# Kernel tuning notes

Hardware: AMD Instinct MI355X
Metric: run time of the kernel (lower is better)

The kernel has to match this reference:

```python
import jax, jax.numpy as jnp
import numpy as np

B, L, U, G, H = 64, 110, 768, 512, 256
WP = WF = 10
NSP = 2
R = 2 * NSP * NSP      # 8 relation types
NB = 30                # RGCN num_bases
FF = 2048              # torch TransformerEncoderLayer default dim_feedforward
TAG = 7
N = B * L
NEG = -1e9


def _build_edges():
    # static windowed edge structure (all dialogues have length L)
    js, ks = [], []
    for j in range(L):
        for k in range(max(0, j - WP), min(L - 1, j + WF) + 1):
            js.append(j); ks.append(k)
    j = np.asarray(js, np.int32); k = np.asarray(ks, np.int32)
    c = (j >= k).astype(np.int32)  # edge_type suffix: '0' if j<k else '1'
    off = (np.arange(B, dtype=np.int32) * L)[:, None]
    src = (j[None, :] + off).reshape(-1)
    dst = (k[None, :] + off).reshape(-1)
    return src, dst, np.tile(k, B), np.tile(c, B)


def _ln(x, g, b):
    m = x.mean(-1, keepdims=True)
    v = ((x - m) ** 2).mean(-1, keepdims=True)
    return (x - m) / jnp.sqrt(v + 1e-5) * g + b


def _core(x, in_proj_w, in_proj_b, out_proj_w, out_proj_b, ln1_g, ln1_b,
          ff1_w, ff1_b, ff2_w, ff2_b, ln2_g, ln2_b, to_w, to_b, att_w,
          rgcn_basis, rgcn_comp, rgcn_root, rgcn_bias,
          gc_rel_w, gc_rel_b, gc_root_w, clf1_w, clf1_b, clf2_w, clf2_b,
          speaker, src, dst, k_local, cflag):
    # --- SeqContext: 1-layer, 1-head post-norm transformer (eval mode) ---
    qkv = x @ in_proj_w.T + in_proj_b
    q, kk, v = jnp.split(qkv, 3, axis=-1)
    attn = jax.nn.softmax(jnp.einsum('bqd,bkd->bqk', q, kk) / jnp.sqrt(jnp.float32(U)), -1)
    a = jnp.einsum('bqk,bkd->bqd', attn, v) @ out_proj_w.T + out_proj_b
    h = _ln(x + a, ln1_g, ln1_b)
    ff = jax.nn.relu(h @ ff1_w.T + ff1_b) @ ff2_w.T + ff2_b
    h = _ln(h + ff, ln2_g, ln2_b)
    feats = h @ to_w.T + to_b                      # (B, L, G) node features

    # --- EdgeAtt: windowed softmax attention, score[j,k] = x_j^T W x_k ---
    scores = jnp.einsum('bjd,de,bke->bjk', feats, att_w, feats)
    rel = jnp.arange(L)[None, :] - jnp.arange(L)[:, None]
    mask = (rel >= -WP) & (rel <= WF)
    alpha = jax.nn.softmax(jnp.where(mask[None], scores, NEG), -1)  # (B, L, L)

    xf = feats.reshape(N, G)
    edge_norm = alpha.reshape(N, L)[src, k_local]   # alpha[b, j, k] per edge

    # --- edge types from speakers: idx = (s1*NSP + s2)*2 + c ---
    sp = speaker.reshape(N)
    etype = (sp[src] * NSP + sp[dst]) * 2 + cflag

    # --- RGCNConv: basis decomposition, per-(node, relation) mean + root ---
    w_rel = jnp.einsum('rb,bgh->rgh', rgcn_comp, rgcn_basis)   # (R, G, H)
    xproj = jnp.einsum('ng,rgh->rnh', xf, w_rel)               # (R, N, H)
    msg = xproj[etype, src]                                    # (E, H)
    seg = dst * R + etype
    cnt = jax.ops.segment_sum(jnp.ones_like(edge_norm), seg, num_segments=N * R)
    msg = msg / jnp.maximum(cnt[seg], 1.0)[:, None]
    h1 = jax.ops.segment_sum(msg, dst, num_segments=N) + xf @ rgcn_root + rgcn_bias

    # --- GraphConv: sum-aggregate edge-weighted neighbors + root ---
    agg = jax.ops.segment_sum(edge_norm[:, None] * h1[src], dst, num_segments=N)
    h2 = agg @ gc_rel_w.T + gc_rel_b + h1 @ gc_root_w.T

    # --- Classifier (dropout inactive in eval) ---
    z = jnp.concatenate([xf, h2], axis=-1)
    return jax.nn.relu(z @ clf1_w.T + clf1_b) @ clf2_w.T + clf2_b  # (N, TAG)


def setup_inputs():
    key = jax.random.key(0)
    ks = jax.random.split(key, 16)
    def rn(i, shape, scale=0.02):
        return jax.random.normal(ks[i], shape, jnp.float32) * scale
    src, dst, k_local, cflag = _build_edges()
    return {
        'x': jax.random.normal(ks[0], (B, L, U), jnp.float32),
        'in_proj_w': rn(1, (3 * U, U)), 'in_proj_b': jnp.zeros((3 * U,), jnp.float32),
        'out_proj_w': rn(2, (U, U)), 'out_proj_b': jnp.zeros((U,), jnp.float32),
        'ln1_g': jnp.ones((U,), jnp.float32), 'ln1_b': jnp.zeros((U,), jnp.float32),
        'ff1_w': rn(3, (FF, U)), 'ff1_b': jnp.zeros((FF,), jnp.float32),
        'ff2_w': rn(4, (U, FF)), 'ff2_b': jnp.zeros((U,), jnp.float32),
        'ln2_g': jnp.ones((U,), jnp.float32), 'ln2_b': jnp.zeros((U,), jnp.float32),
        'to_w': rn(5, (G, U)), 'to_b': jnp.zeros((G,), jnp.float32),
        'att_w': rn(6, (G, G), 2.0 / (G + G)),
        'rgcn_basis': rn(7, (NB, G, H)), 'rgcn_comp': rn(8, (R, NB), 0.2),
        'rgcn_root': rn(9, (G, H)), 'rgcn_bias': jnp.zeros((H,), jnp.float32),
        'gc_rel_w': rn(10, (H, H)), 'gc_rel_b': jnp.zeros((H,), jnp.float32),
        'gc_root_w': rn(11, (H, H)),
        'clf1_w': rn(12, (H, G + H)), 'clf1_b': jnp.zeros((H,), jnp.float32),
        'clf2_w': rn(13, (TAG, H)), 'clf2_b': jnp.zeros((TAG,), jnp.float32),
        'speaker': jax.random.randint(ks[14], (B, L), 0, NSP, jnp.int32),
        'src': jnp.asarray(src), 'dst': jnp.asarray(dst),
        'k_local': jnp.asarray(k_local), 'cflag': jnp.asarray(cflag),
        'length': L,
    }


def reference(x, in_proj_w, in_proj_b, out_proj_w, out_proj_b, ln1_g, ln1_b,
              ff1_w, ff1_b, ff2_w, ff2_b, ln2_g, ln2_b, to_w, to_b, att_w,
              rgcn_basis, rgcn_comp, rgcn_root, rgcn_bias,
              gc_rel_w, gc_rel_b, gc_root_w, clf1_w, clf1_b, clf2_w, clf2_b,
              speaker, src, dst, k_local, cflag, length):
    return _core(x, in_proj_w, in_proj_b, out_proj_w, out_proj_b, ln1_g, ln1_b,
                 ff1_w, ff1_b, ff2_w, ff2_b, ln2_g, ln2_b, to_w, to_b, att_w,
                 rgcn_basis, rgcn_comp, rgcn_root, rgcn_bias,
                 gc_rel_w, gc_rel_b, gc_root_w, clf1_w, clf1_b, clf2_w, clf2_b,
                 speaker, src, dst, k_local, cflag)
```

## Files before the change

kernel.cpp:

```cpp
#include <hip/hip_runtime.h>
#include <hip/hip_bf16.h>
#include <math.h>

#define L_   110
#define B_   64
#define N_   7040
#define U_   768
#define G_   512
#define H_   256
#define FF_  2048
#define EPB_ 2200
#define NC_  2816

typedef __attribute__((ext_vector_type(4))) float f32x4;
typedef __attribute__((ext_vector_type(8))) short bf16x8;

__device__ __forceinline__ ushort f2b(float f) {
  union { __hip_bfloat16 h; ushort u; } cv;
  cv.h = __float2bfloat16(f);
  return cv.u;
}
__device__ __forceinline__ float b2f(ushort u) {
  union { float f; unsigned int i; } cv; cv.i = ((unsigned int)u) << 16; return cv.f;
}

__device__ __forceinline__ int edge_prefix(int j) {
  if (j <= 10)  return j * 11 + (j * (j - 1)) / 2;
  if (j <= 100) return 155 + (j - 10) * 21;
  return 2045 + ((141 - j) * (j - 100)) / 2;
}

struct Segs7 { const float* in[7]; ushort* out[7]; int n4[7]; };

__global__ __launch_bounds__(256)
void cvtprep_kernel(Segs7 s, const float* __restrict__ rb,
                    const float* __restrict__ rel, const float* __restrict__ root,
                    float* __restrict__ bias, ushort* __restrict__ gccat)
{
  const int seg = blockIdx.y;
  if (seg < 7) {
    const int n4 = s.n4[seg];
    const float* __restrict__ in = s.in[seg];
    ushort* __restrict__ out = s.out[seg];
    for (int i = blockIdx.x * 256 + threadIdx.x; i < n4; i += gridDim.x * 256) {
      float4 v = ((const float4*)in)[i];
      ushort4 o;
      o.x = f2b(v.x); o.y = f2b(v.y); o.z = f2b(v.z); o.w = f2b(v.w);
      ((ushort4*)out)[i] = o;
    }
  } else {
    const int i = blockIdx.x * 256 + threadIdx.x;
    if (i < NC_) {
      bias[i] = (i < 2560) ? 0.f : rb[i - 2560];
    } else if (i < NC_ + 65536) {
      const int j = i - NC_;
      const int r = j >> 8, c = j & 255;
      gccat[(size_t)r * 512 + c]       = f2b(rel[j]);
      gccat[(size_t)r * 512 + 256 + c] = f2b(root[j]);
    }
  }
}

__global__ __launch_bounds__(256)
void tcvt3_kernel(const float* __restrict__ attw, const float* __restrict__ wrelTmp,
                  const float* __restrict__ root, ushort* __restrict__ combw)
{
  const int z = blockIdx.z;
  const float* in;
  ushort* out;
  int C;
  if (z == 0)      { in = attw; out = combw; C = 512; }
  else if (z <= 8) { if (blockIdx.x >= 8) return;
                     in = wrelTmp + (size_t)(z - 1) * 512 * 256;
                     out = combw + (size_t)(512 + (z - 1) * 256) * 512; C = 256; }
  else             { if (blockIdx.x >= 8) return;
                     in = root; out = combw + (size_t)2560 * 512; C = 256; }
  __shared__ float t[32][33];
  const int r0 = blockIdx.y * 32, c0 = blockIdx.x * 32;
  const int tx = threadIdx.x & 31, ty = threadIdx.x >> 5;
  for (int i = ty; i < 32; i += 8)
    t[i][tx] = in[(size_t)(r0 + i) * C + c0 + tx];
  __syncthreads();
  for (int i = ty; i < 32; i += 8)
    out[(size_t)(c0 + i) * 512 + r0 + tx] = f2b(t[tx][i]);
}

__global__ __launch_bounds__(256)
void wrel_kernel(const float* __restrict__ basis, const float* __restrict__ comp,
                 float* __restrict__ wrel)
{
  __shared__ float cs[240];
  const int tid = threadIdx.x;
  if (tid < 240) cs[tid] = comp[tid];
  __syncthreads();
  const int gh = blockIdx.x * 256 + tid;
  float acc[8] = {};
  for (int bb = 0; bb < 30; ++bb) {
    float v = basis[(size_t)bb * (G_ * H_) + gh];
#pragma unroll
    for (int r = 0; r < 8; ++r) acc[r] = fmaf(cs[r * 30 + bb], v, acc[r]);
  }
#pragma unroll
  for (int r = 0; r < 8; ++r) wrel[(size_t)r * (G_ * H_) + gh] = acc[r];
}

template<bool BIAS, bool RELU>
__global__ __launch_bounds__(256)
void mgemm_kernel(const ushort* __restrict__ A, const ushort* __restrict__ B,
                  const float* __restrict__ bias, ushort* __restrict__ Cb,
                  int K, int lda, int ldb, int ldc)
{
  __shared__ ushort sA[128 * 64];
  __shared__ ushort sB[128 * 64];
  const int tid = threadIdx.x;
  const int w = tid >> 6, l = tid & 63;

  const int gx = gridDim.x;
  const int nwg = gx * gridDim.y;
  const int lid = blockIdx.y * gx + blockIdx.x;
  const int q = nwg >> 3, r = nwg & 7;
  const int xcd = lid & 7, pos = lid >> 3;
  const int nlid = (xcd < r ? xcd * (q + 1) : r * (q + 1) + (xcd - r) * q) + pos;
  const int m0 = (nlid / gx) * 128, n0 = (nlid % gx) * 128;

  const int srow = l >> 3, sg = l & 7, rbase = w * 32;
  const int wr = w >> 1, wc = w & 1;
  const int lrow = l & 15, lk = l >> 4;
  const int xm = (l & 7) << 4;
  const int kb0 = (lk * 16) ^ xm;
  int aoff[4], boff[4];
#pragma unroll
  for (int i = 0; i < 4; ++i) {
    aoff[i] = (wr * 64 + i * 16 + lrow) * 128 + kb0;
    boff[i] = (wc * 64 + i * 16 + lrow) * 128 + kb0;
  }

  f32x4 acc[4][4];
#pragma unroll
  for (int i = 0; i < 4; ++i)
#pragma unroll
    for (int j = 0; j < 4; ++j) acc[i][j] = (f32x4){0.f, 0.f, 0.f, 0.f};

#define STAGE(k0)                                                              \
  {                                                                            \
    _Pragma("unroll")                                                          \
    for (int i = 0; i < 4; ++i) {                                              \
      const int trow = rbase + i * 8 + srow;                                   \
      const int koff = (sg * 8) ^ ((trow & 7) << 3);                           \
      const ushort* ga = A + (size_t)(m0 + trow) * lda + (k0) + koff;          \
      const ushort* gb = B + (size_t)(n0 + trow) * ldb + (k0) + koff;          \
      __builtin_amdgcn_global_load_lds(                                        \
          (const __attribute__((address_space(1))) void*)ga,                   \
          (__attribute__((address_space(3))) void*)&sA[(rbase + i * 8) * 64],  \
          16, 0, 0);                                                           \
      __builtin_amdgcn_global_load_lds(                                        \
          (const __attribute__((address_space(1))) void*)gb,                   \
          (__attribute__((address_space(3))) void*)&sB[(rbase + i * 8) * 64],  \
          16, 0, 0);                                                           \
    }                                                                          \
  }

  STAGE(0)
  for (int kt = 0;;) {
    __syncthreads();
#pragma unroll
    for (int h = 0; h < 2; ++h) {
      const int hx = h * 64;
      bf16x8 af[4], bfr[4];
#pragma unroll
      for (int i = 0; i < 4; ++i) {
        af[i]  = *(const bf16x8*)&sA[(aoff[i] ^ hx) >> 1];
        bfr[i] = *(const bf16x8*)&sB[(boff[i] ^ hx) >> 1];
      }
#pragma unroll
      for (int mi = 0; mi < 4; ++mi)
#pragma unroll
        for (int ni = 0; ni < 4; ++ni)
          acc[mi][ni] = __builtin_amdgcn_mfma_f32_16x16x32_bf16(
              af[mi], bfr[ni], acc[mi][ni], 0, 0, 0);
    }
    kt += 64;
    if (kt >= K) break;
    __syncthreads();
    STAGE(kt)
  }
#undef STAGE

  const int orow = m0 + wr * 64 + lk * 4;
  const int ocol = n0 + wc * 64 + lrow;
#pragma unroll
  for (int mi = 0; mi < 4; ++mi) {
#pragma unroll
    for (int r2 = 0; r2 < 4; ++r2) {
      const int row = orow + mi * 16 + r2;
#pragma unroll
      for (int ni = 0; ni < 4; ++ni) {
        const int col = ocol + ni * 16;
        float v = acc[mi][ni][r2];
        if constexpr (BIAS) v += bias[col];
        if constexpr (RELU) v = fmaxf(v, 0.f);
        Cb[(size_t)row * ldc + col] = f2b(v);
      }
    }
  }
}

template<bool BIAS, bool RELU>
__global__ __launch_bounds__(256)
void mgemm64_kernel(const ushort* __restrict__ A, const ushort* __restrict__ B,
                    const float* __restrict__ bias, ushort* __restrict__ Cb,
                    int K, int lda, int ldb, int ldc)
{
  __shared__ ushort sA[128 * 64];
  __shared__ ushort sB[64 * 64];
  const int tid = threadIdx.x;
  const int w = tid >> 6, l = tid & 63;

  const int gx = gridDim.x;
  const int nwg = gx * gridDim.y;
  const int lid = blockIdx.y * gx + blockIdx.x;
  const int q = nwg >> 3, r = nwg & 7;
  const int xcd = lid & 7, pos = lid >> 3;
  const int nlid = (xcd < r ? xcd * (q + 1) : r * (q + 1) + (xcd - r) * q) + pos;
  const int m0 = (nlid / gx) * 128, n0 = (nlid % gx) * 64;

  const int srow = l >> 3, sg = l & 7;
  const int lrow = l & 15, lk = l >> 4;
  const int xm = (l & 7) << 4;
  const int kb0 = (lk * 16) ^ xm;
  int aoff[2], boff[4];
#pragma unroll
  for (int i = 0; i < 2; ++i) aoff[i] = (w * 32 + i * 16 + lrow) * 128 + kb0;
#pragma unroll
  for (int i = 0; i < 4; ++i) boff[i] = (i * 16 + lrow) * 128 + kb0;

  f32x4 acc[2][4];
#pragma unroll
  for (int i = 0; i < 2; ++i)
#pragma unroll
    for (int j = 0; j < 4; ++j) acc[i][j] = (f32x4){0.f, 0.f, 0.f, 0.f};

#define STAGE64(k0)                                                            \
  {                                                                            \
    _Pragma("unroll")                                                          \
    for (int i = 0; i < 4; ++i) {                                              \
      const int trow = w * 32 + i * 8 + srow;                                  \
      const int koff = (sg * 8) ^ ((trow & 7) << 3);                           \
      const ushort* ga = A + (size_t)(m0 + trow) * lda + (k0) + koff;          \
      __builtin_amdgcn_global_load_lds(                                        \
          (const __attribute__((address_space(1))) void*)ga,                   \
          (__attribute__((address_space(3))) void*)&sA[(w * 32 + i * 8) * 64], \
          16, 0, 0);                                                           \
    }                                                                          \
    _Pragma("unroll")                                                          \
    for (int i = 0; i < 2; ++i) {                                              \
      const int trow = w * 16 + i * 8 + srow;                                  \
      const int koff = (sg * 8) ^ ((trow & 7) << 3);                           \
      const ushort* gb = B + (size_t)(n0 + trow) * ldb + (k0) + koff;          \
      __builtin_amdgcn_global_load_lds(                                        \
          (const __attribute__((address_space(1))) void*)gb,                   \
          (__attribute__((address_space(3))) void*)&sB[(w * 16 + i * 8) * 64], \
          16, 0, 0);                                                           \
    }                                                                          \
  }

  STAGE64(0)
  for (int kt = 0;;) {
    __syncthreads();
#pragma unroll
    for (int h = 0; h < 2; ++h) {
      const int hx = h * 64;
      bf16x8 af[2], bfr[4];
#pragma unroll
      for (int i = 0; i < 2; ++i) af[i] = *(const bf16x8*)&sA[(aoff[i] ^ hx) >> 1];
#pragma unroll
      for (int i = 0; i < 4; ++i) bfr[i] = *(const bf16x8*)&sB[(boff[i] ^ hx) >> 1];
#pragma unroll
      for (int mi = 0; mi < 2; ++mi)
#pragma unroll
        for (int ni = 0; ni < 4; ++ni)
          acc[mi][ni] = __builtin_amdgcn_mfma_f32_16x16x32_bf16(
              af[mi], bfr[ni], acc[mi][ni], 0, 0, 0);
    }
    kt += 64;
    if (kt >= K) break;
    __syncthreads();
    STAGE64(kt)
  }
#undef STAGE64

  const int orow = m0 + w * 32 + lk * 4;
  const int ocol = n0 + lrow;
#pragma unroll
  for (int mi = 0; mi < 2; ++mi) {
#pragma unroll
    for (int r2 = 0; r2 < 4; ++r2) {
      const int row = orow + mi * 16 + r2;
#pragma unroll
      for (int ni = 0; ni < 4; ++ni) {
        const int col = ocol + ni * 16;
        float v = acc[mi][ni][r2];
        if constexpr (BIAS) v += bias[col];
        if constexpr (RELU) v = fmaxf(v, 0.f);
        Cb[(size_t)row * ldc + col] = f2b(v);
      }
    }
  }
}

__global__ __launch_bounds__(256)
void vtrans_kernel(const ushort* __restrict__ qkvb, ushort* __restrict__ vt)
{
  __shared__ ushort t[32][33];
  const int b = blockIdx.z;
  const int r0 = blockIdx.y * 32;
  const int c0 = blockIdx.x * 32;
  const int tx = threadIdx.x & 31, ty = threadIdx.x >> 5;
  for (int i = ty; i < 32; i += 8) {
    const int r = r0 + i;
    t[i][tx] = (r < L_) ? qkvb[((size_t)(b * L_) + r) * 2304 + 1536 + c0 + tx]
                        : (ushort)0;
  }
  __syncthreads();
  for (int i = ty; i < 32; i += 8)
    vt[((size_t)b * 768 + c0 + i) * 128 + r0 + tx] = t[tx][i];
}

__global__ __launch_bounds__(256)
void attnM_kernel(const ushort* __restrict__ qkvb, const ushort* __restrict__ vt,
                  ushort* __restrict__ ctxb)
{
  const int wg = blockIdx.x;
  const int xcd = wg & 7, slot = wg >> 3;
  const int b = xcd * 8 + slot / 7;
  const int qr0 = (slot % 7) * 16;
  const int tid = threadIdx.x, w = tid >> 6, l = tid & 63;
  __shared__ float  sS[16 * 128];
  __shared__ ushort sP[16 * 128];
  const int lrow = l & 15, lq = l >> 4;

  const ushort* Qbase = qkvb + ((size_t)(b * L_) + qr0 + lrow) * 2304 + lq * 8;
  f32x4 accS[2] = {{0.f,0.f,0.f,0.f},{0.f,0.f,0.f,0.f}};
  const int nf0 = w * 2;
  for (int k0 = 0; k0 < 768; k0 += 32) {
    bf16x8 aq = *(const bf16x8*)(Qbase + k0);
#pragma unroll
    for (int f = 0; f < 2; ++f) {
      const int nf = nf0 + f;
      if (nf < 7) {
        const ushort* Kp = qkvb + ((size_t)(b * L_) + nf * 16 + lrow) * 2304
                         + 768 + k0 + lq * 8;
        bf16x8 bk = *(const bf16x8*)Kp;
        accS[f] = __builtin_amdgcn_mfma_f32_16x16x32_bf16(aq, bk, accS[f], 0, 0, 0);
      }
    }
  }
  const float scale = 0.03608439182435161f;
#pragma unroll
  for (int f = 0; f < 2; ++f) {
    const int nf = nf0 + f;
    if (nf < 7) {
#pragma unroll
      for (int r = 0; r < 4; ++r)
        sS[(lq * 4 + r) * 128 + nf * 16 + lrow] = accS[f][r] * scale;
    }
  }
  __syncthreads();

  {
    const int row = w * 4 + lq;
    const int c0 = lrow;
    float m = -1e30f;
    for (int c = c0; c < L_; c += 16) m = fmaxf(m, sS[row * 128 + c]);
#pragma unroll
    for (int off = 8; off; off >>= 1) m = fmaxf(m, __shfl_xor(m, off));
    float pv[7];
    float sum = 0.f;
#pragma unroll
    for (int i = 0; i < 7; ++i) {
      const int c = c0 + i * 16;
      float e = (c < L_) ? __expf(sS[row * 128 + c] - m) : 0.f;
      pv[i] = e; sum += e;
    }
#pragma unroll
    for (int off = 8; off; off >>= 1) sum += __shfl_xor(sum, off);
    const float inv = 1.f / sum;
#pragma unroll
    for (int i = 0; i < 8; ++i) {
      const int c = c0 + i * 16;
      ushort pb = (i < 7 && c < L_) ? f2b(pv[i < 7 ? i : 0] * inv) : (ushort)0;
      const int g = (c >> 3) ^ (row & 7);
      sP[row * 128 + g * 8 + (c & 7)] = pb;
    }
  }
  __syncthreads();

  f32x4 accO[12];
#pragma unroll
  for (int i = 0; i < 12; ++i) accO[i] = (f32x4){0.f, 0.f, 0.f, 0.f};
#pragma unroll
  for (int ks = 0; ks < 4; ++ks) {
    const int k = ks * 32 + lq * 8;
    const int g = (k >> 3) ^ (lrow & 7);
    bf16x8 ap = *(const bf16x8*)&sP[lrow * 128 + g * 8];
#pragma unroll
    for (int i = 0; i < 12; ++i) {
      const int col = w * 192 + i * 16 + lrow;
      bf16x8 bv = *(const bf16x8*)(vt + ((size_t)b * 768 + col) * 128 + k);
      accO[i] = __builtin_amdgcn_mfma_f32_16x16x32_bf16(ap, bv, accO[i], 0, 0, 0);
    }
  }
#pragma unroll
  for (int i = 0; i < 12; ++i) {
    const int col = w * 192 + i * 16 + lrow;
#pragma unroll
    for (int r = 0; r < 4; ++r) {
      const int row = qr0 + lq * 4 + r;
      if (row < L_)
        ctxb[((size_t)b * L_ + row) * 768 + col] = f2b(accO[i][r]);
    }
  }
}

template<bool AF32>
__global__ __launch_bounds__(256)
void ln_kernel(const float* __restrict__ Af, const ushort* __restrict__ Ab,
               const ushort* __restrict__ Bres,
               const float* __restrict__ g, const float* __restrict__ beta,
               ushort* __restrict__ outb)
{
  const int row = blockIdx.x, tid = threadIdx.x;
  const ushort* bp = Bres + (size_t)row * U_;
  float a0, a1, a2;
  if constexpr (AF32) {
    const float* ap = Af + (size_t)row * U_;
    a0 = ap[tid]; a1 = ap[tid + 256]; a2 = ap[tid + 512];
  } else {
    const ushort* ap = Ab + (size_t)row * U_;
    a0 = b2f(ap[tid]); a1 = b2f(ap[tid + 256]); a2 = b2f(ap[tid + 512]);
  }
  float v0 = a0 + b2f(bp[tid]);
  float v1 = a1 + b2f(bp[tid + 256]);
  float v2 = a2 + b2f(bp[tid + 512]);
  float s = v0 + v1 + v2, sq = v0 * v0 + v1 * v1 + v2 * v2;
  __shared__ float red[8];
#pragma unroll
  for (int off = 32; off; off >>= 1) { s += __shfl_xor(s, off); sq += __shfl_xor(sq, off); }
  const int wave = tid >> 6, lane = tid & 63;
  if (lane == 0) { red[wave] = s; red[4 + wave] = sq; }
  __syncthreads();
  if (tid == 0) {
    float ts = red[0] + red[1] + red[2] + red[3];
    float tq = red[4] + red[5] + red[6] + red[7];
    float m = ts * (1.f / 768.f);
    float var = tq * (1.f / 768.f) - m * m;
    red[0] = m; red[1] = 1.f / sqrtf(var + 1e-5f);
  }
  __syncthreads();
  const float m = red[0], inv = red[1];
  ushort* ob = outb + (size_t)row * U_;
  ob[tid]       = f2b((v0 - m) * inv * g[tid]       + beta[tid]);
  ob[tid + 256] = f2b((v1 - m) * inv * g[tid + 256] + beta[tid + 256]);
  ob[tid + 512] = f2b((v2 - m) * inv * g[tid + 512] + beta[tid + 512]);
}

__global__ __launch_bounds__(256)
void graphfront_kernel(const ushort* __restrict__ combo, const ushort* __restrict__ fcat,
                       const int* __restrict__ speaker,
                       ushort* __restrict__ catb, float* __restrict__ edge_norm)
{
  const int tid = threadIdx.x;
  if (blockIdx.x < N_ / 8) {
    const int n = blockIdx.x * 8 + (tid >> 5);
    const int lane = tid & 31;
    const int b = n / L_, k = n - b * L_;
    const int j0 = max(0, k - 10), j1 = min(L_ - 1, k + 10);
    const int spk = speaker[n];
    float inv[4];
    {
      int cn[4] = {0, 0, 0, 0};
      for (int j = j0; j <= j1; ++j)
        cn[speaker[b * L_ + j] * 2 + (j >= k ? 1 : 0)]++;
#pragma unroll
      for (int q = 0; q < 4; ++q) inv[q] = cn[q] ? 1.f / (float)cn[q] : 0.f;
    }
    float acc[8] = {};
    for (int j = j0; j <= j1; ++j) {
      const int spj = speaker[b * L_ + j];
      const int c = (j >= k) ? 1 : 0;
      const int et = (spj * 2 + spk) * 2 + c;
      const float w = inv[spj * 2 + c];
      bf16x8 v = *(const bf16x8*)&combo[(size_t)(b * L_ + j) * NC_ + 512 + et * 256 + lane * 8];
#pragma unroll
      for (int i = 0; i < 8; ++i) acc[i] = fmaf(b2f((ushort)v[i]), w, acc[i]);
    }
    bf16x8 rt = *(const bf16x8*)&combo[(size_t)n * NC_ + 2560 + lane * 8];
    bf16x8 o;
#pragma unroll
    for (int i = 0; i < 8; ++i) o[i] = (short)f2b(acc[i] + b2f((ushort)rt[i]));
    *(bf16x8*)&catb[(size_t)n * 512 + 256 + lane * 8] = o;
  } else {
    const int bj = blockIdx.x - N_ / 8;
    const int b = bj / L_, j = bj - b * L_;
    const int k0 = max(0, j - 10), k1 = min(L_ - 1, j + 10);
    __shared__ float s[32];
    const int wave = tid >> 6, lane = tid & 63;
    float tr[8];
    {
      bf16x8 tv = *(const bf16x8*)&combo[(size_t)bj * NC_ + lane * 8];
#pragma unroll
      for (int i = 0; i < 8; ++i) tr[i] = b2f((ushort)tv[i]);
    }
    for (int k = k0 + wave; k <= k1; k += 4) {
      bf16x8 v = *(const bf16x8*)&fcat[(size_t)(b * L_ + k) * 768 + lane * 8];
      float sc = 0.f;
#pragma unroll
      for (int i = 0; i < 8; ++i) sc = fmaf(b2f((ushort)v[i]), tr[i], sc);
#pragma unroll
      for (int off = 32; off; off >>= 1) sc += __shfl_xor(sc, off);
      if (lane == 0) s[k - k0] = sc;
    }
    __syncthreads();
    if (tid == 0) {
      const int W = k1 - k0 + 1;
      float m = -1e30f;
      for (int t = 0; t < W; ++t) m = fmaxf(m, s[t]);
      float sum = 0.f;
      for (int t = 0; t < W; ++t) { float e = __expf(s[t] - m); s[t] = e; sum += e; }
      const float inv = 1.f / sum;
      const int base = b * EPB_ + edge_prefix(j);
      for (int t = 0; t < W; ++t) edge_norm[base + t] = s[t] * inv;
    }
  }
}

__global__ __launch_bounds__(256)
void gcn_gather2_kernel(const float* __restrict__ edge_norm,
                        ushort* __restrict__ catb)
{
  const int tid = threadIdx.x;
  const int n = blockIdx.x * 8 + (tid >> 5);
  const int lane = tid & 31;
  const int b = n / L_, k = n - b * L_;
  const int j0 = max(0, k - 10), j1 = min(L_ - 1, k + 10);
  float acc[8] = {};
  for (int j = j0; j <= j1; ++j) {
    const float w = edge_norm[b * EPB_ + edge_prefix(j) + (k - max(0, j - 10))];
    bf16x8 v = *(const bf16x8*)&catb[(size_t)(b * L_ + j) * 512 + 256 + lane * 8];
#pragma unroll
    for (int i = 0; i < 8; ++i) acc[i] = fmaf(b2f((ushort)v[i]), w, acc[i]);
  }
  bf16x8 o;
#pragma unroll
  for (int i = 0; i < 8; ++i) o[i] = (short)f2b(acc[i]);
  *(bf16x8*)&catb[(size_t)n * 512 + lane * 8] = o;
}

__global__ __launch_bounds__(256)
void clf2_kernel(const ushort* __restrict__ hid, const float* __restrict__ w,
                 const float* __restrict__ bias, float* __restrict__ out)
{
  __shared__ float wsm[7 * H_];
  const int tid = threadIdx.x;
  for (int i = tid; i < 7 * H_; i += 256) wsm[i] = w[i];
  __syncthreads();
  const int idx = blockIdx.x * 256 + threadIdx.x;
  if (idx < N_ * 7) {
    const int n = idx / 7, t = idx - n * 7;
    const ushort* hp = hid + (size_t)n * H_;
    const float* wp = wsm + t * H_;
    float acc = bias[t];
    for (int d0 = 0; d0 < H_; d0 += 8) {
      bf16x8 v = *(const bf16x8*)(hp + d0);
#pragma unroll
      for (int i = 0; i < 8; ++i) acc = fmaf(b2f((ushort)v[i]), wp[d0 + i], acc);
    }
    out[idx] = acc;
  }
}

extern "C" void kernel_launch(void* const* d_in, const int* in_sizes, int n_in,
                              void* d_out, int out_size, void* d_ws, size_t ws_size,
                              hipStream_t stream)
{
  const float* x          = (const float*)d_in[0];
  const float* in_proj_w  = (const float*)d_in[1];
  const float* in_proj_b  = (const float*)d_in[2];
  const float* out_proj_w = (const float*)d_in[3];
  const float* out_proj_b = (const float*)d_in[4];
  const float* ln1_g      = (const float*)d_in[5];
  const float* ln1_b      = (const float*)d_in[6];
  const float* ff1_w      = (const float*)d_in[7];
  const float* ff1_b      = (const float*)d_in[8];
  const float* ff2_w      = (const float*)d_in[9];
  const float* ff2_b      = (const float*)d_in[10];
  const float* ln2_g      = (const float*)d_in[11];
  const float* ln2_b      = (const float*)d_in[12];
  const float* to_w       = (const float*)d_in[13];
  const float* to_b       = (const float*)d_in[14];
  const float* att_w      = (const float*)d_in[15];
  const float* rgcn_basis = (const float*)d_in[16];
  const float* rgcn_comp  = (const float*)d_in[17];
  const float* rgcn_root  = (const float*)d_in[18];
  const float* rgcn_bias  = (const float*)d_in[19];
  const float* gc_rel_w   = (const float*)d_in[20];
  const float* gc_rel_b   = (const float*)d_in[21];
  const float* gc_root_w  = (const float*)d_in[22];
  const float* clf1_w     = (const float*)d_in[23];
  const float* clf1_b     = (const float*)d_in[24];
  const float* clf2_w     = (const float*)d_in[25];
  const float* clf2_b     = (const float*)d_in[26];
  const int*   speaker    = (const int*)d_in[27];
  float* out = (float*)d_out;
  char* p = (char*)d_ws;

  float*  R1f    = (float*)p;
  ushort* R1b    = (ushort*)p;
  p += (size_t)N_ * 2304 * 4;
  ushort* aprojB = (ushort*)p;
  ushort* ffoB   = aprojB;
  float*  en     = (float*)(p + (size_t)N_ * 512 * 4);
  p += (size_t)N_ * 768 * 4;
  ushort* vt    = (ushort*)p;
  ushort* hidB  = (ushort*)p;
  p += (size_t)N_ * 768 * 4;
  ushort* xb    = (ushort*)p;
  ushort* ctxb  = xb;
  p += (size_t)N_ * 768 * 2;
  ushort* hb    = (ushort*)p;
  ushort* catb  = hb;
  p += (size_t)N_ * 768 * 2;
  ushort* fcat  = (ushort*)p; p += (size_t)N_ * 768 * 2;
  ushort* in_projb = (ushort*)p; p += (size_t)2304 * 768 * 2;
  ushort* out_projb= (ushort*)p; p += (size_t)768 * 768 * 2;
  ushort* ff1b     = (ushort*)p; p += (size_t)2048 * 768 * 2;
  ushort* ff2b     = (ushort*)p; p += (size_t)768 * 2048 * 2;
  ushort* tob      = (ushort*)p; p += (size_t)512 * 768 * 2;
  ushort* combw    = (ushort*)p; p += (size_t)NC_ * 512 * 2;
  ushort* gccat    = (ushort*)p; p += (size_t)256 * 512 * 2;
  ushort* clf1b16  = (ushort*)p; p += (size_t)256 * 768 * 2;
  float*  bias_comb= (float*)p;  p += NC_ * 4;
  float*  wrelTmp  = R1f;

  Segs7 segs;
  segs.in[0] = x;          segs.out[0] = xb;        segs.n4[0] = N_ * 768 / 4;
  segs.in[1] = in_proj_w;  segs.out[1] = in_projb;  segs.n4[1] = 2304 * 768 / 4;
  segs.in[2] = out_proj_w; segs.out[2] = out_projb; segs.n4[2] = 768 * 768 / 4;
  segs.in[3] = ff1_w;      segs.out[3] = ff1b;      segs.n4[3] = 2048 * 768 / 4;
  segs.in[4] = ff2_w;      segs.out[4] = ff2b;      segs.n4[4] = 768 * 2048 / 4;
  segs.in[5] = to_w;       segs.out[5] = tob;       segs.n4[5] = 512 * 768 / 4;
  segs.in[6] = clf1_w;     segs.out[6] = clf1b16;   segs.n4[6] = 256 * 768 / 4;
  cvtprep_kernel<<<dim3(768, 8), 256, 0, stream>>>(
      segs, rgcn_bias, gc_rel_w, gc_root_w, bias_comb, gccat);
  wrel_kernel<<<512, 256, 0, stream>>>(rgcn_basis, rgcn_comp, wrelTmp);
  tcvt3_kernel<<<dim3(16, 16, 10), 256, 0, stream>>>(att_w, wrelTmp, rgcn_root, combw);

  mgemm_kernel<true, false><<<dim3(18, 55), 256, 0, stream>>>(
      xb, in_projb, in_proj_b, R1b, 768, 768, 768, 2304);
  vtrans_kernel<<<dim3(24, 4, 64), 256, 0, stream>>>(R1b, vt);
  attnM_kernel<<<448, 256, 0, stream>>>(R1b, vt, ctxb);
  mgemm64_kernel<true, false><<<dim3(12, 55), 256, 0, stream>>>(
      ctxb, out_projb, out_proj_b, aprojB, 768, 768, 768, 768);
  ln_kernel<true><<<N_, 256, 0, stream>>>(x, nullptr, aprojB, ln1_g, ln1_b, hb);
  mgemm_kernel<true, true><<<dim3(16, 55), 256, 0, stream>>>(
      hb, ff1b, ff1_b, R1b, 768, 768, 768, 2048);
  mgemm64_kernel<true, false><<<dim3(12, 55), 256, 0, stream>>>(
      R1b, ff2b, ff2_b, ffoB, 2048, 2048, 2048, 768);
  ln_kernel<false><<<N_, 256, 0, stream>>>(nullptr, hb, ffoB, ln2_g, ln2_b, hb);
  mgemm64_kernel<true, false><<<dim3(8, 55), 256, 0, stream>>>(
      hb, tob, to_b, fcat, 768, 768, 768, 768);
  mgemm_kernel<true, false><<<dim3(22, 55), 256, 0, stream>>>(
      fcat, combw, bias_comb, R1b, 512, 768, 512, NC_);
  graphfront_kernel<<<N_ / 8 + N_, 256, 0, stream>>>(R1b, fcat, speaker, catb, en);
  gcn_gather2_kernel<<<N_ / 8, 256, 0, stream>>>(en, catb);
  mgemm64_kernel<true, false><<<dim3(4, 55), 256, 0, stream>>>(
      catb, gccat, gc_rel_b, fcat + 512, 512, 512, 512, 768);
  mgemm64_kernel<true, true><<<dim3(4, 55), 256, 0, stream>>>(
      fcat, clf1b16, clf1_b, hidB, 768, 768, 768, 256);
  clf2_kernel<<<(N_ * 7 + 255) / 256, 256, 0, stream>>>(hidB, clf2_w, clf2_b, out);
}
```

Baseline: 303.7 us.

## Fuse RGCN basis combination with transpose, widen vtrans accesses, use bf16 residual in LN1

Merges the basis-combination kernel and the transpose/convert kernel into one kernel that computes the relation weights per 32x32 tile and writes them transposed as bf16 directly, dropping an fp32 temporary round trip and a launch. The V transpose kernel now moves two bf16 values per access with padded shared memory. LN1 reads the bf16 copy of x instead of fp32 x, so it loads less data but the residual loses precision. The ctx buffer is moved to fcat so the bf16 x copy stays intact until LN1 reads it.

```diff
diff --git a/kernel.cpp b/kernel.cpp
--- a/kernel.cpp
+++ b/kernel.cpp
@@ -62,46 +62,48 @@
 }
 
 __global__ __launch_bounds__(256)
-void tcvt3_kernel(const float* __restrict__ attw, const float* __restrict__ wrelTmp,
-                  const float* __restrict__ root, ushort* __restrict__ combw)
-{
-  const int z = blockIdx.z;
-  const float* in;
-  ushort* out;
-  int C;
-  if (z == 0)      { in = attw; out = combw; C = 512; }
-  else if (z <= 8) { if (blockIdx.x >= 8) return;
-                     in = wrelTmp + (size_t)(z - 1) * 512 * 256;
-                     out = combw + (size_t)(512 + (z - 1) * 256) * 512; C = 256; }
-  else             { if (blockIdx.x >= 8) return;
-                     in = root; out = combw + (size_t)2560 * 512; C = 256; }
+void wrelt_kernel(const float* __restrict__ attw, const float* __restrict__ basis,
+                  const float* __restrict__ comp, const float* __restrict__ root,
+                  ushort* __restrict__ combw)
+{
+  const int tx = threadIdx.x & 31, ty = threadIdx.x >> 5;
   __shared__ float t[32][33];
-  const int r0 = blockIdx.y * 32, c0 = blockIdx.x * 32;
-  const int tx = threadIdx.x & 31, ty = threadIdx.x >> 5;
-  for (int i = ty; i < 32; i += 8)
-    t[i][tx] = in[(size_t)(r0 + i) * C + c0 + tx];
-  __syncthreads();
-  for (int i = ty; i < 32; i += 8)
-    out[(size_t)(c0 + i) * 512 + r0 + tx] = f2b(t[tx][i]);
-}
-
-__global__ __launch_bounds__(256)
-void wrel_kernel(const float* __restrict__ basis, const float* __restrict__ comp,
-                 float* __restrict__ wrel)
-{
-  __shared__ float cs[240];
-  const int tid = threadIdx.x;
-  if (tid < 240) cs[tid] = comp[tid];
-  __syncthreads();
-  const int gh = blockIdx.x * 256 + tid;
-  float acc[8] = {};
-  for (int bb = 0; bb < 30; ++bb) {
-    float v = basis[(size_t)bb * (G_ * H_) + gh];
-#pragma unroll
-    for (int r = 0; r < 8; ++r) acc[r] = fmaf(cs[r * 30 + bb], v, acc[r]);
-  }
-#pragma unroll
-  for (int r = 0; r < 8; ++r) wrel[(size_t)r * (G_ * H_) + gh] = acc[r];
+  if (blockIdx.z == 0) {
+    const int r0 = blockIdx.y * 32, c0 = blockIdx.x * 32;
+    for (int i = ty; i < 32; i += 8)
+      t[i][tx] = attw[(size_t)(r0 + i) * 512 + c0 + tx];
+    __syncthreads();
+    for (int i = ty; i < 32; i += 8)
+      combw[(size_t)(c0 + i) * 512 + r0 + tx] = f2b(t[tx][i]);
+  } else {
+    if (blockIdx.y >= 8) return;
+    const int g0 = blockIdx.x * 32, h0 = blockIdx.y * 32;
+    __shared__ float cs[240];
+    if (threadIdx.x < 240) cs[threadIdx.x] = comp[threadIdx.x];
+    for (int i = ty; i < 32; i += 8)
+      t[i][tx] = root[(size_t)(g0 + i) * 256 + h0 + tx];
+    __syncthreads();
+    for (int i = ty; i < 32; i += 8)
+      combw[(size_t)(2560 + h0 + i) * 512 + g0 + tx] = f2b(t[tx][i]);
+    float acc[8][4] = {};
+    for (int bb = 0; bb < 30; ++bb) {
+      const float* bp = basis + (size_t)bb * (G_ * H_);
+#pragma unroll
+      for (int k = 0; k < 4; ++k) {
+        float v = bp[(size_t)(g0 + ty + 8 * k) * 256 + h0 + tx];
+#pragma unroll
+        for (int r = 0; r < 8; ++r) acc[r][k] = fmaf(cs[r * 30 + bb], v, acc[r][k]);
+      }
+    }
+    for (int r = 0; r < 8; ++r) {
+      __syncthreads();
+#pragma unroll
+      for (int k = 0; k < 4; ++k) t[ty + 8 * k][tx] = acc[r][k];
+      __syncthreads();
+      for (int i = ty; i < 32; i += 8)
+        combw[(size_t)(512 + r * 256 + h0 + i) * 512 + g0 + tx] = f2b(t[tx][i]);
+    }
+  }
 }
 
 template<bool BIAS, bool RELU>
@@ -311,19 +313,24 @@
 __global__ __launch_bounds__(256)
 void vtrans_kernel(const ushort* __restrict__ qkvb, ushort* __restrict__ vt)
 {
-  __shared__ ushort t[32][33];
+  __shared__ ushort t[32][34];
   const int b = blockIdx.z;
   const int r0 = blockIdx.y * 32;
   const int c0 = blockIdx.x * 32;
-  const int tx = threadIdx.x & 31, ty = threadIdx.x >> 5;
-  for (int i = ty; i < 32; i += 8) {
-    const int r = r0 + i;
-    t[i][tx] = (r < L_) ? qkvb[((size_t)(b * L_) + r) * 2304 + 1536 + c0 + tx]
-                        : (ushort)0;
+  const int tid = threadIdx.x;
+  for (int e = tid; e < 512; e += 256) {
+    const int ri = e >> 4, ci2 = (e & 15) * 2;
+    ushort2 v = make_ushort2(0, 0);
+    if (r0 + ri < L_)
+      v = *(const ushort2*)&qkvb[((size_t)(b * L_) + r0 + ri) * 2304 + 1536 + c0 + ci2];
+    t[ri][ci2] = v.x; t[ri][ci2 + 1] = v.y;
   }
   __syncthreads();
-  for (int i = ty; i < 32; i += 8)
-    vt[((size_t)b * 768 + c0 + i) * 128 + r0 + tx] = t[tx][i];
+  for (int e = tid; e < 512; e += 256) {
+    const int ci = e >> 4, ri2 = (e & 15) * 2;
+    ushort2 o = make_ushort2(t[ri2][ci], t[ri2 + 1][ci]);
+    *(ushort2*)&vt[((size_t)b * 768 + c0 + ci) * 128 + r0 + ri2] = o;
+  }
 }
 
 __global__ __launch_bounds__(256)
@@ -422,26 +429,17 @@
   }
 }
 
-template<bool AF32>
-__global__ __launch_bounds__(256)
-void ln_kernel(const float* __restrict__ Af, const ushort* __restrict__ Ab,
-               const ushort* __restrict__ Bres,
+__global__ __launch_bounds__(256)
+void ln_kernel(const ushort* __restrict__ Ab, const ushort* __restrict__ Bres,
                const float* __restrict__ g, const float* __restrict__ beta,
                ushort* __restrict__ outb)
 {
   const int row = blockIdx.x, tid = threadIdx.x;
+  const ushort* ap = Ab + (size_t)row * U_;
   const ushort* bp = Bres + (size_t)row * U_;
-  float a0, a1, a2;
-  if constexpr (AF32) {
-    const float* ap = Af + (size_t)row * U_;
-    a0 = ap[tid]; a1 = ap[tid + 256]; a2 = ap[tid + 512];
-  } else {
-    const ushort* ap = Ab + (size_t)row * U_;
-    a0 = b2f(ap[tid]); a1 = b2f(ap[tid + 256]); a2 = b2f(ap[tid + 512]);
-  }
-  float v0 = a0 + b2f(bp[tid]);
-  float v1 = a1 + b2f(bp[tid + 256]);
-  float v2 = a2 + b2f(bp[tid + 512]);
+  float v0 = b2f(ap[tid])       + b2f(bp[tid]);
+  float v1 = b2f(ap[tid + 256]) + b2f(bp[tid + 256]);
+  float v2 = b2f(ap[tid + 512]) + b2f(bp[tid + 512]);
   float s = v0 + v1 + v2, sq = v0 * v0 + v1 * v1 + v2 * v2;
   __shared__ float red[8];
 #pragma unroll
@@ -614,7 +612,6 @@
   float* out = (float*)d_out;
   char* p = (char*)d_ws;
 
-  float*  R1f    = (float*)p;
   ushort* R1b    = (ushort*)p;
   p += (size_t)N_ * 2304 * 4;
   ushort* aprojB = (ushort*)p;
@@ -625,12 +622,13 @@
   ushort* hidB  = (ushort*)p;
   p += (size_t)N_ * 768 * 4;
   ushort* xb    = (ushort*)p;
-  ushort* ctxb  = xb;
   p += (size_t)N_ * 768 * 2;
   ushort* hb    = (ushort*)p;
   ushort* catb  = hb;
   p += (size_t)N_ * 768 * 2;
-  ushort* fcat  = (ushort*)p; p += (size_t)N_ * 768 * 2;
+  ushort* fcat  = (ushort*)p;
+  ushort* ctxb  = fcat;
+  p += (size_t)N_ * 768 * 2;
   ushort* in_projb = (ushort*)p; p += (size_t)2304 * 768 * 2;
   ushort* out_projb= (ushort*)p; p += (size_t)768 * 768 * 2;
   ushort* ff1b     = (ushort*)p; p += (size_t)2048 * 768 * 2;
@@ -640,7 +638,6 @@
   ushort* gccat    = (ushort*)p; p += (size_t)256 * 512 * 2;
   ushort* clf1b16  = (ushort*)p; p += (size_t)256 * 768 * 2;
   float*  bias_comb= (float*)p;  p += NC_ * 4;
-  float*  wrelTmp  = R1f;
 
   Segs7 segs;
   segs.in[0] = x;          segs.out[0] = xb;        segs.n4[0] = N_ * 768 / 4;
@@ -652,8 +649,8 @@
   segs.in[6] = clf1_w;     segs.out[6] = clf1b16;   segs.n4[6] = 256 * 768 / 4;
   cvtprep_kernel<<<dim3(768, 8), 256, 0, stream>>>(
       segs, rgcn_bias, gc_rel_w, gc_root_w, bias_comb, gccat);
-  wrel_kernel<<<512, 256, 0, stream>>>(rgcn_basis, rgcn_comp, wrelTmp);
-  tcvt3_kernel<<<dim3(16, 16, 10), 256, 0, stream>>>(att_w, wrelTmp, rgcn_root, combw);
+  wrelt_kernel<<<dim3(16, 16, 2), 256, 0, stream>>>(
+      att_w, rgcn_basis, rgcn_comp, rgcn_root, combw);
 
   mgemm_kernel<true, false><<<dim3(18, 55), 256, 0, stream>>>(
       xb, in_projb, in_proj_b, R1b, 768, 768, 768, 2304);
@@ -661,12 +658,12 @@
   attnM_kernel<<<448, 256, 0, stream>>>(R1b, vt, ctxb);
   mgemm64_kernel<true, false><<<dim3(12, 55), 256, 0, stream>>>(
       ctxb, out_projb, out_proj_b, aprojB, 768, 768, 768, 768);
-  ln_kernel<true><<<N_, 256, 0, stream>>>(x, nullptr, aprojB, ln1_g, ln1_b, hb);
+  ln_kernel<<<N_, 256, 0, stream>>>(xb, aprojB, ln1_g, ln1_b, hb);
   mgemm_kernel<true, true><<<dim3(16, 55), 256, 0, stream>>>(
       hb, ff1b, ff1_b, R1b, 768, 768, 768, 2048);
   mgemm64_kernel<true, false><<<dim3(12, 55), 256, 0, stream>>>(
       R1b, ff2b, ff2_b, ffoB, 2048, 2048, 2048, 768);
-  ln_kernel<false><<<N_, 256, 0, stream>>>(nullptr, hb, ffoB, ln2_g, ln2_b, hb);
+  ln_kernel<<<N_, 256, 0, stream>>>(hb, ffoB, ln2_g, ln2_b, hb);
   mgemm64_kernel<true, false><<<dim3(8, 55), 256, 0, stream>>>(
       hb, tob, to_b, fcat, 768, 768, 768, 768);
   mgemm_kernel<true, false><<<dim3(22, 55), 256, 0, stream>>>(
```

New measurement: 300.7 us. About the same (-1.0%).
